# Kernel tuning notes

Hardware: AMD Instinct MI355X
Metric: run time of the kernel (lower is better)

## Reference

```python
import jax, jax.numpy as jnp
import numpy as np

NUM_TOKENS = 131072
N_EXPERTS = 256
N_GROUP = 8
TOPK_GROUP = 4
TOP_K = 8
ROUTED_SCALING = 2.5


def setup_inputs() -> dict:
    key = jax.random.key(0)
    k1, k2 = jax.random.split(key)
    router_logits = jax.random.normal(k1, (NUM_TOKENS, N_EXPERTS), dtype=jnp.float32)
    correction_bias = jax.random.normal(k2, (N_EXPERTS,), dtype=jnp.float32) * 0.1
    return {"router_logits": router_logits, "correction_bias": correction_bias}


def reference(router_logits, correction_bias):
    T = router_logits.shape[0]
    eg = N_EXPERTS // N_GROUP  # experts per group = 32

    scores = jax.nn.sigmoid(router_logits).astype(jnp.float32)          # [T, 256]
    scores_for_choice = scores + correction_bias[None, :]                # [T, 256]

    # group score = sum of top-2 corrected scores within each group
    grp = scores_for_choice.reshape(T, N_GROUP, eg)                      # [T, 8, 32]
    top2, _ = jax.lax.top_k(grp, 2)                                      # [T, 8, 2]
    group_scores = top2.sum(axis=-1)                                     # [T, 8]

    # pick top groups, build expert-level mask
    _, group_idx = jax.lax.top_k(group_scores, TOPK_GROUP)               # [T, 4]
    rows = jnp.arange(T)[:, None]
    group_mask = jnp.zeros_like(group_scores).at[rows, group_idx].set(1.0)  # [T, 8]
    score_mask = jnp.repeat(group_mask, eg, axis=-1)                     # [T, 256]

    masked_scores = jnp.where(score_mask > 0, scores_for_choice, 0.0)
    _, topk_indices = jax.lax.top_k(masked_scores, TOP_K)                # [T, 8]

    topk_weights = jnp.take_along_axis(scores, topk_indices, axis=1)     # [T, 8]
    denom = topk_weights.sum(axis=-1, keepdims=True) + 1e-20
    topk_weights = topk_weights / denom * ROUTED_SCALING
    return (topk_indices, topk_weights)
```

## Files before the change

kernel.cpp:

```cpp
#include <hip/hip_runtime.h>
#include <math.h>


constexpr int N_EXPERTS  = 256;
constexpr int N_GROUP    = 8;
constexpr int EG         = 32;
constexpr int TOPK_GROUP = 4;
constexpr int TOP_K      = 8;
constexpr int BLOCK      = 512;
constexpr int TPB_TOK    = BLOCK / N_GROUP;

typedef unsigned int u32;
typedef unsigned long long u64;

__device__ __forceinline__ u32 fmono(float f) {
  const u32 u = __float_as_uint(f);
  return u ^ ((u32)((int)u >> 31) | 0x80000000u);
}
__device__ __forceinline__ float fmono_inv(u32 m) {
  const u32 u = (m & 0x80000000u) ? (m ^ 0x80000000u) : ~m;
  return __uint_as_float(u);
}
__device__ __forceinline__ u64 mkkey(float v, int idx) {
  return ((u64)fmono(v) << 32) | (u32)(255 - idx);
}
__device__ __forceinline__ int key_idx(u64 k) { return 255 - (int)(k & 0xFFu); }
__device__ __forceinline__ float key_val(u64 k) { return fmono_inv((u32)(k >> 32)); }

__device__ __forceinline__ float recip_nr(float d) {
  float r = __builtin_amdgcn_rcpf(d);
  r = __builtin_fmaf(__builtin_fmaf(-d, r, 1.0f), r, r);
  r = __builtin_fmaf(__builtin_fmaf(-d, r, 1.0f), r, r);
  return r;
}

__device__ __forceinline__ void kswap(u64& a, u64& b) {
  const bool sw = b > a;
  const u64 t = sw ? b : a;
  b = sw ? a : b;
  a = t;
}

__device__ __forceinline__ void sort8(u64 (&k)[8]) {
  kswap(k[0], k[1]); kswap(k[2], k[3]); kswap(k[4], k[5]); kswap(k[6], k[7]);
  kswap(k[0], k[2]); kswap(k[1], k[3]); kswap(k[4], k[6]); kswap(k[5], k[7]);
  kswap(k[1], k[2]); kswap(k[5], k[6]);
  kswap(k[0], k[4]); kswap(k[1], k[5]); kswap(k[2], k[6]); kswap(k[3], k[7]);
  kswap(k[2], k[4]); kswap(k[3], k[5]);
  kswap(k[1], k[2]); kswap(k[3], k[4]); kswap(k[5], k[6]);
}

__device__ __forceinline__ void merge8(u64 (&A)[8], const u64 (&B)[8]) {
  u64 R[8];
#pragma unroll
  for (int i = 0; i < 8; ++i) {
    const bool a = A[i] >= B[7 - i];
    R[i] = a ? A[i] : B[7 - i];
  }
  kswap(R[0], R[4]); kswap(R[1], R[5]); kswap(R[2], R[6]); kswap(R[3], R[7]);
  kswap(R[0], R[2]); kswap(R[1], R[3]); kswap(R[4], R[6]); kswap(R[5], R[7]);
  kswap(R[0], R[1]); kswap(R[2], R[3]); kswap(R[4], R[5]); kswap(R[6], R[7]);
#pragma unroll
  for (int i = 0; i < 8; ++i) A[i] = R[i];
}

__global__ __launch_bounds__(BLOCK) void deepseek_topk_router_r9(
    const float* __restrict__ logits,
    const float* __restrict__ bias,
    float* __restrict__ out,
    int T) {
  __shared__ __align__(16) float gsb[BLOCK];
  __shared__ u64 kbuf[N_GROUP][BLOCK];

  const int tid = threadIdx.x;
  const int id  = blockIdx.x * BLOCK + tid;
  const int t   = id >> 3;
  const int q   = id & 7;

  const float4* row4 =
      reinterpret_cast<const float4*>(logits + (size_t)t * N_EXPERTS + q * EG);
  const float4* b4 = reinterpret_cast<const float4*>(bias + q * EG);

  float4 x[8];
#pragma unroll
  for (int u = 0; u < 8; ++u) x[u] = row4[u];
  float4 bb[8];
#pragma unroll
  for (int u = 0; u < 8; ++u) bb[u] = b4[u];

  u64 K[8];
#pragma unroll
  for (int c = 0; c < 4; ++c) {
    u64 C[8];
    const float xs[8] = {x[2*c].x, x[2*c].y, x[2*c].z, x[2*c].w,
                         x[2*c+1].x, x[2*c+1].y, x[2*c+1].z, x[2*c+1].w};
    const float bs[8] = {bb[2*c].x, bb[2*c].y, bb[2*c].z, bb[2*c].w,
                         bb[2*c+1].x, bb[2*c+1].y, bb[2*c+1].z, bb[2*c+1].w};
#pragma unroll
    for (int j = 0; j < 8; ++j) {
      const float e = expf(-xs[j]);
      const float s = recip_nr(1.0f + e);
      C[j] = mkkey(s + bs[j], q * EG + c * 8 + j);
    }
    sort8(C);
    if (c == 0) {
#pragma unroll
      for (int j = 0; j < 8; ++j) K[j] = C[j];
    } else {
      merge8(K, C);
    }
  }

  gsb[tid] = key_val(K[0]) + key_val(K[1]);
#pragma unroll
  for (int k = 0; k < 8; ++k) kbuf[k][tid] = K[k];
  __syncthreads();
  if (tid >= TPB_TOK) return;

  const int j   = tid;
  const int tok = blockIdx.x * TPB_TOK + j;

  const float4* gp = reinterpret_cast<const float4*>(&gsb[8 * j]);
  const float4 ga = gp[0], gb = gp[1];
  const float g[N_GROUP] = {ga.x, ga.y, ga.z, ga.w, gb.x, gb.y, gb.z, gb.w};

  int s0 = 0, s1 = 0, s2 = 0, s3 = 0, cnt = 0;
#pragma unroll
  for (int h = 0; h < N_GROUP; ++h) {
    int rank = 0;
#pragma unroll
    for (int m = 0; m < N_GROUP; ++m)
      rank += (m < h) ? (g[m] >= g[h] ? 1 : 0) : (g[m] > g[h] ? 1 : 0);
    const bool pick = (rank < TOPK_GROUP);
    s0 = (pick && cnt == 0) ? h : s0;
    s1 = (pick && cnt == 1) ? h : s1;
    s2 = (pick && cnt == 2) ? h : s2;
    s3 = (pick && cnt == 3) ? h : s3;
    cnt += pick ? 1 : 0;
  }

  u64 A[8], B[8];
  const int base = 8 * j;
#pragma unroll
  for (int k = 0; k < 8; ++k) A[k] = kbuf[k][base + s0];
#pragma unroll
  for (int k = 0; k < 8; ++k) B[k] = kbuf[k][base + s1];
  merge8(A, B);
#pragma unroll
  for (int k = 0; k < 8; ++k) B[k] = kbuf[k][base + s2];
  merge8(A, B);
#pragma unroll
  for (int k = 0; k < 8; ++k) B[k] = kbuf[k][base + s3];
  merge8(A, B);

  float fi[8], sv[8];
  float sum = 0.0f;
#pragma unroll
  for (int k = 0; k < TOP_K; ++k) {
    const int idx = key_idx(A[k]);
    const float c = key_val(A[k]);
    sv[k] = c - bias[idx];
    fi[k] = (float)idx;
    sum += sv[k];
  }
  const float scale = 2.5f / (sum + 1e-20f);

  float4* oi = reinterpret_cast<float4*>(out) + (size_t)tok * 2;
  oi[0] = make_float4(fi[0], fi[1], fi[2], fi[3]);
  oi[1] = make_float4(fi[4], fi[5], fi[6], fi[7]);
  float4* ow = reinterpret_cast<float4*>(out + (size_t)T * TOP_K) + (size_t)tok * 2;
  ow[0] = make_float4(sv[0] * scale, sv[1] * scale, sv[2] * scale, sv[3] * scale);
  ow[1] = make_float4(sv[4] * scale, sv[5] * scale, sv[6] * scale, sv[7] * scale);
}

extern "C" void kernel_launch(void* const* d_in, const int* in_sizes, int n_in,
                              void* d_out, int out_size, void* d_ws, size_t ws_size,
                              hipStream_t stream) {
  const float* logits = (const float*)d_in[0];
  const float* bias   = (const float*)d_in[1];
  float* out = (float*)d_out;
  const int T = in_sizes[0] / N_EXPERTS;
  const int blocks = T / TPB_TOK;
  deepseek_topk_router_r9<<<blocks, BLOCK, 0, stream>>>(logits, bias, out, T);
}
```

Measured before the change: 207.2 us.

## Replace shared-memory group reduction with intra-octet shuffles and staggered loads

The cross-group stage now runs with wave shuffles within each 8-lane token octet instead of shared memory. Each lane computes its group's rank and masks its top-8 list if the group is not picked, then a 3-step xor butterfly merge yields the final top-8. The bias is staged once per block in LDS, logits are loaded in staggered chunks to overlap with sorting, and the block shrinks to 256 threads. This removes the large kbuf LDS footprint and the single-thread serial tail, in exchange for more shuffle traffic and redundant merges across all 8 lanes.

```diff
diff --git a/kernel.cpp b/kernel.cpp
--- a/kernel.cpp
+++ b/kernel.cpp
@@ -7,8 +7,7 @@
 constexpr int EG         = 32;
 constexpr int TOPK_GROUP = 4;
 constexpr int TOP_K      = 8;
-constexpr int BLOCK      = 512;
-constexpr int TPB_TOK    = BLOCK / N_GROUP;
+constexpr int BLOCK      = 256;
 
 typedef unsigned int u32;
 typedef unsigned long long u64;
@@ -64,113 +63,134 @@
   for (int i = 0; i < 8; ++i) A[i] = R[i];
 }
 
-__global__ __launch_bounds__(BLOCK) void deepseek_topk_router_r9(
+__device__ __forceinline__ u64 shfl_xor_u64(u64 v, int m) {
+  const int lo = __shfl_xor((int)(u32)v, m, 8);
+  const int hi = __shfl_xor((int)(u32)(v >> 32), m, 8);
+  return ((u64)(u32)hi << 32) | (u32)lo;
+}
+
+__device__ __forceinline__ void chunk_sort(u64 (&K)[8], const float4 xa,
+                                           const float4 xb, const float4 ba,
+                                           const float4 bv, const int idx0,
+                                           const bool first) {
+  u64 C[8];
+  const float xs[8] = {xa.x, xa.y, xa.z, xa.w, xb.x, xb.y, xb.z, xb.w};
+  const float bs[8] = {ba.x, ba.y, ba.z, ba.w, bv.x, bv.y, bv.z, bv.w};
+#pragma unroll
+  for (int j = 0; j < 8; ++j) {
+    const float e = expf(-xs[j]);
+    const float s = recip_nr(1.0f + e);
+    C[j] = mkkey(s + bs[j], idx0 + j);
+  }
+  sort8(C);
+  if (first) {
+#pragma unroll
+    for (int j = 0; j < 8; ++j) K[j] = C[j];
+  } else {
+    merge8(K, C);
+  }
+}
+
+__global__ __launch_bounds__(BLOCK) void deepseek_topk_router_r14(
     const float* __restrict__ logits,
     const float* __restrict__ bias,
     float* __restrict__ out,
     int T) {
-  __shared__ __align__(16) float gsb[BLOCK];
-  __shared__ u64 kbuf[N_GROUP][BLOCK];
+  __shared__ __align__(16) float bias_lds[N_GROUP][36];
 
   const int tid = threadIdx.x;
   const int id  = blockIdx.x * BLOCK + tid;
   const int t   = id >> 3;
   const int q   = id & 7;
 
-  const float4* row4 =
+  const float4* rp =
       reinterpret_cast<const float4*>(logits + (size_t)t * N_EXPERTS + q * EG);
-  const float4* b4 = reinterpret_cast<const float4*>(bias + q * EG);
-
-  float4 x[8];
-#pragma unroll
-  for (int u = 0; u < 8; ++u) x[u] = row4[u];
-  float4 bb[8];
-#pragma unroll
-  for (int u = 0; u < 8; ++u) bb[u] = b4[u];
+
+  float4 a0 = rp[0], a1 = rp[1];
+  float4 b0 = rp[2], b1 = rp[3];
+
+  if (tid < N_EXPERTS) bias_lds[tid >> 5][tid & 31] = bias[tid];
+  __syncthreads();
+  const float4* brow = reinterpret_cast<const float4*>(bias_lds[q]);
+  const int qbase = q * EG;
 
   u64 K[8];
-#pragma unroll
-  for (int c = 0; c < 4; ++c) {
-    u64 C[8];
-    const float xs[8] = {x[2*c].x, x[2*c].y, x[2*c].z, x[2*c].w,
-                         x[2*c+1].x, x[2*c+1].y, x[2*c+1].z, x[2*c+1].w};
-    const float bs[8] = {bb[2*c].x, bb[2*c].y, bb[2*c].z, bb[2*c].w,
-                         bb[2*c+1].x, bb[2*c+1].y, bb[2*c+1].z, bb[2*c+1].w};
-#pragma unroll
-    for (int j = 0; j < 8; ++j) {
-      const float e = expf(-xs[j]);
-      const float s = recip_nr(1.0f + e);
-      C[j] = mkkey(s + bs[j], q * EG + c * 8 + j);
+  chunk_sort(K, a0, a1, brow[0], brow[1], qbase + 0,  true);
+  a0 = rp[4]; a1 = rp[5];
+  chunk_sort(K, b0, b1, brow[2], brow[3], qbase + 8,  false);
+  b0 = rp[6]; b1 = rp[7];
+  chunk_sort(K, a0, a1, brow[4], brow[5], qbase + 16, false);
+  chunk_sort(K, b0, b1, brow[6], brow[7], qbase + 24, false);
+
+  const float gq = key_val(K[0]) + key_val(K[1]);
+  const float p1 = __shfl_xor(gq, 1, 8);
+  const bool o1 = (q & 1) != 0;
+  const float e0 = o1 ? p1 : gq;
+  const float e1 = o1 ? gq : p1;
+  const float f0 = __shfl_xor(e0, 2, 8);
+  const float f1 = __shfl_xor(e1, 2, 8);
+  const bool o2 = (q & 2) != 0;
+  const float d0 = o2 ? f0 : e0;
+  const float d1 = o2 ? f1 : e1;
+  const float d2 = o2 ? e0 : f0;
+  const float d3 = o2 ? e1 : f1;
+  const float h0 = __shfl_xor(d0, 4, 8);
+  const float h1 = __shfl_xor(d1, 4, 8);
+  const float h2 = __shfl_xor(d2, 4, 8);
+  const float h3 = __shfl_xor(d3, 4, 8);
+  const bool o4 = (q & 4) != 0;
+  const float g0 = o4 ? h0 : d0;
+  const float g1 = o4 ? h1 : d1;
+  const float g2 = o4 ? h2 : d2;
+  const float g3 = o4 ? h3 : d3;
+  const float g4 = o4 ? d0 : h0;
+  const float g5 = o4 ? d1 : h1;
+  const float g6 = o4 ? d2 : h2;
+  const float g7 = o4 ? d3 : h3;
+
+  int rank = 0;
+#define RANK_TERM(m, gm) \
+  rank += ((m) < q) ? ((gm) >= gq ? 1 : 0) : ((((m) > q) && ((gm) > gq)) ? 1 : 0);
+  RANK_TERM(0, g0) RANK_TERM(1, g1) RANK_TERM(2, g2) RANK_TERM(3, g3)
+  RANK_TERM(4, g4) RANK_TERM(5, g5) RANK_TERM(6, g6) RANK_TERM(7, g7)
+#undef RANK_TERM
+  const bool pick = (rank < TOPK_GROUP);
+
+#pragma unroll
+  for (int k = 0; k < 8; ++k) K[k] = pick ? K[k] : 0ULL;
+
+  u64 P[8];
+#pragma unroll
+  for (int k = 0; k < 8; ++k) P[k] = shfl_xor_u64(K[k], 1);
+  merge8(K, P);
+#pragma unroll
+  for (int k = 0; k < 8; ++k) P[k] = shfl_xor_u64(K[k], 2);
+  merge8(K, P);
+#pragma unroll
+  for (int k = 0; k < 8; ++k) P[k] = shfl_xor_u64(K[k], 4);
+  merge8(K, P);
+
+  if (q == 0) {
+    float fi[8], sv[8];
+    float sum = 0.0f;
+#pragma unroll
+    for (int k = 0; k < TOP_K; ++k) {
+      const int idx = key_idx(K[k]);
+      const float c = key_val(K[k]);
+      sv[k] = c - bias_lds[idx >> 5][idx & 31];
+      fi[k] = (float)idx;
+      sum += sv[k];
     }
-    sort8(C);
-    if (c == 0) {
-#pragma unroll
-      for (int j = 0; j < 8; ++j) K[j] = C[j];
-    } else {
-      merge8(K, C);
-    }
-  }
-
-  gsb[tid] = key_val(K[0]) + key_val(K[1]);
-#pragma unroll
-  for (int k = 0; k < 8; ++k) kbuf[k][tid] = K[k];
-  __syncthreads();
-  if (tid >= TPB_TOK) return;
-
-  const int j   = tid;
-  const int tok = blockIdx.x * TPB_TOK + j;
-
-  const float4* gp = reinterpret_cast<const float4*>(&gsb[8 * j]);
-  const float4 ga = gp[0], gb = gp[1];
-  const float g[N_GROUP] = {ga.x, ga.y, ga.z, ga.w, gb.x, gb.y, gb.z, gb.w};
-
-  int s0 = 0, s1 = 0, s2 = 0, s3 = 0, cnt = 0;
-#pragma unroll
-  for (int h = 0; h < N_GROUP; ++h) {
-    int rank = 0;
-#pragma unroll
-    for (int m = 0; m < N_GROUP; ++m)
-      rank += (m < h) ? (g[m] >= g[h] ? 1 : 0) : (g[m] > g[h] ? 1 : 0);
-    const bool pick = (rank < TOPK_GROUP);
-    s0 = (pick && cnt == 0) ? h : s0;
-    s1 = (pick && cnt == 1) ? h : s1;
-    s2 = (pick && cnt == 2) ? h : s2;
-    s3 = (pick && cnt == 3) ? h : s3;
-    cnt += pick ? 1 : 0;
-  }
-
-  u64 A[8], B[8];
-  const int base = 8 * j;
-#pragma unroll
-  for (int k = 0; k < 8; ++k) A[k] = kbuf[k][base + s0];
-#pragma unroll
-  for (int k = 0; k < 8; ++k) B[k] = kbuf[k][base + s1];
-  merge8(A, B);
-#pragma unroll
-  for (int k = 0; k < 8; ++k) B[k] = kbuf[k][base + s2];
-  merge8(A, B);
-#pragma unroll
-  for (int k = 0; k < 8; ++k) B[k] = kbuf[k][base + s3];
-  merge8(A, B);
-
-  float fi[8], sv[8];
-  float sum = 0.0f;
-#pragma unroll
-  for (int k = 0; k < TOP_K; ++k) {
-    const int idx = key_idx(A[k]);
-    const float c = key_val(A[k]);
-    sv[k] = c - bias[idx];
-    fi[k] = (float)idx;
-    sum += sv[k];
-  }
-  const float scale = 2.5f / (sum + 1e-20f);
-
-  float4* oi = reinterpret_cast<float4*>(out) + (size_t)tok * 2;
-  oi[0] = make_float4(fi[0], fi[1], fi[2], fi[3]);
-  oi[1] = make_float4(fi[4], fi[5], fi[6], fi[7]);
-  float4* ow = reinterpret_cast<float4*>(out + (size_t)T * TOP_K) + (size_t)tok * 2;
-  ow[0] = make_float4(sv[0] * scale, sv[1] * scale, sv[2] * scale, sv[3] * scale);
-  ow[1] = make_float4(sv[4] * scale, sv[5] * scale, sv[6] * scale, sv[7] * scale);
+    const float scale = 2.5f / (sum + 1e-20f);
+
+    float4* oi = reinterpret_cast<float4*>(out) + (size_t)t * 2;
+    oi[0] = make_float4(fi[0], fi[1], fi[2], fi[3]);
+    oi[1] = make_float4(fi[4], fi[5], fi[6], fi[7]);
+    float4* ow =
+        reinterpret_cast<float4*>(out + (size_t)T * TOP_K) + (size_t)t * 2;
+    ow[0] = make_float4(sv[0] * scale, sv[1] * scale, sv[2] * scale, sv[3] * scale);
+    ow[1] = make_float4(sv[4] * scale, sv[5] * scale, sv[6] * scale, sv[7] * scale);
+  }
 }
 
 extern "C" void kernel_launch(void* const* d_in, const int* in_sizes, int n_in,
@@ -180,6 +200,6 @@
   const float* bias   = (const float*)d_in[1];
   float* out = (float*)d_out;
   const int T = in_sizes[0] / N_EXPERTS;
-  const int blocks = T / TPB_TOK;
-  deepseek_topk_router_r9<<<blocks, BLOCK, 0, stream>>>(logits, bias, out, T);
-}
+  const int blocks = (T * N_GROUP) / BLOCK;
+  deepseek_topk_router_r14<<<blocks, BLOCK, 0, stream>>>(logits, bias, out, T);
+}
```

New measurement: 208.5 us. No clear change (+0.6%).
